# Optimization experiments

Measured on AMD Instinct MI355X. Metric: run time of the kernel, lower is better.

The kernel has to match this reference:

```python
import jax, jax.numpy as jnp
import numpy as np

B, CIN, COUT, H, W = 8, 64, 64, 128, 128
DG = 1          # deformable groups
K = 9           # 3x3 kernel taps


def conv2d(x, w, b, pad):
    out = jax.lax.conv_general_dilated(
        x, w, window_strides=(1, 1), padding=[(pad, pad), (pad, pad)],
        dimension_numbers=("NCHW", "OIHW", "NCHW"))
    return out + b[None, :, None, None]


def deform_conv2d(x, offset, w, b, dg):
    """torchvision-style DeformConv2d, 3x3, stride 1, pad 1, zeros outside."""
    Bn, Cin, Hn, Wn = x.shape
    Cout = w.shape[0]
    Cg = Cin // dg
    # offset: [B, 2*dg*K, H, W] -> [B, dg, K, 2, H, W] (dy, dx per tap)
    off = offset.reshape(Bn, dg, K, 2, Hn, Wn)
    ky = jnp.repeat(jnp.arange(3) - 1, 3).astype(x.dtype)   # [K]
    kx = jnp.tile(jnp.arange(3) - 1, 3).astype(x.dtype)     # [K]
    base_y = ky[:, None, None] + jnp.arange(Hn, dtype=x.dtype)[None, :, None]  # [K,H,1]
    base_x = kx[:, None, None] + jnp.arange(Wn, dtype=x.dtype)[None, None, :]  # [K,1,W]
    py = base_y[None, None] + off[:, :, :, 0]   # [B,dg,K,H,W]
    px = base_x[None, None] + off[:, :, :, 1]   # [B,dg,K,H,W]

    xg = x.reshape(Bn, dg, Cg, Hn * Wn)         # grouped, flat spatial
    y0 = jnp.floor(py)
    x0 = jnp.floor(px)
    acc = jnp.zeros((Bn, dg, Cg, K * Hn * Wn), dtype=x.dtype)
    for dy in (0, 1):
        for dx in (0, 1):
            yc = y0 + dy
            xc = x0 + dx
            # bilinear corner weight; |py-yc| <= 1 for the 4 corners
            wgt = (1.0 - jnp.abs(py - yc)) * (1.0 - jnp.abs(px - xc))
            valid = (yc >= 0) & (yc < Hn) & (xc >= 0) & (xc < Wn)
            yi = jnp.clip(yc, 0, Hn - 1).astype(jnp.int32)
            xi = jnp.clip(xc, 0, Wn - 1).astype(jnp.int32)
            idx = (yi * Wn + xi).reshape(Bn, dg, 1, -1)          # [B,dg,1,K*H*W]
            v = jnp.take_along_axis(xg, idx, axis=3)             # [B,dg,Cg,K*H*W]
            acc = acc + v * (wgt * valid.astype(x.dtype)).reshape(Bn, dg, 1, -1)
    sampled = acc.reshape(Bn, dg, Cg, K, Hn, Wn)
    wk = w.reshape(Cout, dg, Cg, K)              # [Cout,dg,Cg,K]
    out = jnp.einsum("bgckhw,ogck->bohw", sampled, wk)
    return out + b[None, :, None, None]


def setup_inputs() -> dict:
    key = jax.random.key(0)
    ks = jax.random.split(key, 12)
    s = 0.05  # weight scale to keep activations bounded through the relu stack
    inp = {
        "x": jax.random.normal(ks[0], (B, CIN, H, W), jnp.float32),
        "of": jax.random.normal(ks[1], (B, 2, H, W), jnp.float32),
        "w1": jax.random.normal(ks[2], (CIN, CIN, 3, 3), jnp.float32) * s,
        "b1": jnp.zeros((CIN,), jnp.float32),
        "w2": jax.random.normal(ks[3], (CIN, CIN, 3, 3), jnp.float32) * s,
        "b2": jnp.zeros((CIN,), jnp.float32),
        "w3": jax.random.normal(ks[4], (CIN, CIN, 3, 3), jnp.float32) * s,
        "b3": jnp.zeros((CIN,), jnp.float32),
        "w_off": jax.random.normal(ks[5], (K * DG * 2, 2, 1, 1), jnp.float32) * 0.1,
        "b_off": jnp.zeros((K * DG * 2,), jnp.float32),
        "w_d": jax.random.normal(ks[6], (COUT, CIN, 3, 3), jnp.float32) * s,
        "b_d": jnp.zeros((COUT,), jnp.float32),
    }
    return inp


def reference(x, of, w1, b1, w2, b2, w3, b3, w_off, b_off, w_d, b_d):
    h = jax.nn.relu(conv2d(x, w1, b1, 1))
    h = jax.nn.relu(conv2d(h, w2, b2, 1))
    h = jax.nn.relu(conv2d(h, w3, b3, 1))
    offset = conv2d(of, w_off, b_off, 0)          # 1x1 offset conv -> [B,18*dg,H,W]
    return deform_conv2d(h, offset, w_d, b_d, DG)
```

## Files before the change

### kernel.cpp

```cpp
#include <hip/hip_runtime.h>
#include <math.h>

#define H_ 128
#define W_ 128
#define B_ 8
#define C_ 64
#define HW_ (H_*W_)
#define PW 130

typedef _Float16 half8 __attribute__((ext_vector_type(8)));
typedef _Float16 half4t __attribute__((ext_vector_type(4)));
typedef float f32x4 __attribute__((ext_vector_type(4)));

__device__ __forceinline__ int clampi(int v, int lo, int hi) {
    return v < lo ? lo : (v > hi ? hi : v);
}

__device__ __forceinline__ void stage16(const _Float16* g, _Float16* l) {
    __builtin_amdgcn_global_load_lds(
        (const __attribute__((address_space(1))) unsigned int*)g,
        (__attribute__((address_space(3))) unsigned int*)l, 16, 0, 0);
}

__global__ __launch_bounds__(256, 4)
void prep_kernel(const float* __restrict__ w1, const float* __restrict__ w2,
                 const float* __restrict__ w3, const float* __restrict__ wd,
                 _Float16* __restrict__ wp,
                 _Float16* __restrict__ z0, _Float16* __restrict__ z1,
                 _Float16* __restrict__ z2,
                 const float* __restrict__ x,  _Float16* __restrict__ xp,
                 const float* __restrict__ of, const float* __restrict__ wof,
                 const float* __restrict__ bof, float* __restrict__ offb) {
    __shared__ float lds[64][129];
    const int blk = blockIdx.x;
    const int tid = threadIdx.x;

    if (blk < 72) {
        int t = blk * 256 + tid;
        if (t >= 4 * 4608) return;
        int set = t / 4608;
        int u   = t - set * 4608;
        const float* w = (set == 0) ? w1 : (set == 1) ? w2 : (set == 2) ? w3 : wd;
        int l  = u & 63;
        int mf = (u >> 6) & 3;
        int ch = (u >> 8) & 1;
        int kk = u >> 9;
        int co   = mf * 16 + (l & 15);
        int cin0 = ch * 32 + (l >> 4) * 8;
        half8 v;
#pragma unroll
        for (int j = 0; j < 8; ++j)
            v[j] = (_Float16)w[((co * C_) + cin0 + j) * 9 + kk];
        *(half8*)(wp + (size_t)set * 36864
                     + (size_t)(((ch * 9 + kk) * 4 + mf) * 64 + l) * 8) = v;
    } else if (blk < 121) {
        int t = (blk - 72) * 256 + tid;
        if (t >= 3 * B_ * 516) return;
        int which = t / (B_ * 516);
        int u = t - which * (B_ * 516);
        _Float16* o = (which == 0) ? z0 : (which == 1) ? z1 : z2;
        int b = u / 516, i = u % 516;
        int yp, xpx;
        if (i < 260) { yp = (i < 130) ? 0 : (PW - 1); xpx = i % 130; }
        else {
            int j = i - 260;
            if (j < 128) { xpx = 0; yp = j + 1; }
            else         { xpx = PW - 1; yp = j - 128 + 1; }
        }
        _Float16* dst = o + ((size_t)(b * PW + yp) * PW + xpx) * C_;
        half8 z = (half8)(_Float16)0.f;
#pragma unroll
        for (int c8 = 0; c8 < 8; ++c8) *(half8*)(dst + c8 * 8) = z;
    } else if (blk < 1145) {
        int bb = blk - 121;
        const int b = bb & 7, y = bb >> 3;
        const int xr = tid & 127, cr = tid >> 7;
        const float* src = x + (size_t)b * C_ * HW_ + y * W_;
#pragma unroll
        for (int i = 0; i < 32; ++i) {
            int c = i * 2 + cr;
            lds[c][xr] = src[(size_t)c * HW_ + xr];
        }
        __syncthreads();
        const int px = tid & 127, hf = tid >> 7;
        _Float16* dst = xp + ((size_t)((b * PW + y + 1) * PW) + px + 1) * C_ + hf * 32;
#pragma unroll
        for (int q = 0; q < 4; ++q) {
            half8 v;
#pragma unroll
            for (int j = 0; j < 8; ++j) v[j] = (_Float16)lds[hf * 32 + q * 8 + j][px];
            *(half8*)(dst + q * 8) = v;
        }
    } else {
        int bb = blk - 1145;
        int bi = bb & 7;
        int p  = (bb >> 3) * 256 + tid;
        float a0 = of[(bi * 2 + 0) * HW_ + p];
        float a1 = of[(bi * 2 + 1) * HW_ + p];
#pragma unroll
        for (int kk = 0; kk < 9; ++kk) {
            float dy = bof[2 * kk]     + wof[(2 * kk) * 2] * a0     + wof[(2 * kk) * 2 + 1] * a1;
            float dx = bof[2 * kk + 1] + wof[(2 * kk + 1) * 2] * a0 + wof[(2 * kk + 1) * 2 + 1] * a1;
            float2 v; v.x = dy; v.y = dx;
            *(float2*)(offb + ((size_t)(bi * 9 + kk) * HW_ + p) * 2) = v;
        }
    }
}

__global__ __launch_bounds__(256, 2)
void conv3x3_mfma(const _Float16* __restrict__ in, const _Float16* __restrict__ wpk,
                  const float* __restrict__ bias, _Float16* __restrict__ outp) {
    __shared__ _Float16 Ash[9 * 4 * 64 * 8];
    __shared__ _Float16 Tile[4 * 4 * 130 * 8];
    const int tid = threadIdx.x;
    const int wv = tid >> 6, l = tid & 63;
    const int l15 = l & 15, lg = l >> 4;
    const int b  = blockIdx.x & 7;
    const int R  = (blockIdx.x >> 3) * 2;
    const int rowi = wv >> 1;
    const int xcol = (wv & 1) * 64;

    f32x4 acc[4][4];
#pragma unroll
    for (int i = 0; i < 4; ++i)
#pragma unroll
        for (int j = 0; j < 4; ++j) acc[i][j] = (f32x4){0.f, 0.f, 0.f, 0.f};

    half8 bf0[4], bf1[4];

#define LOADB(BF, KK)                                                          \
    {                                                                          \
        _Pragma("unroll") for (int nf = 0; nf < 4; ++nf)                       \
            BF[nf] = *(const half8*)(Tile + (size_t)(((rowi + (KK) / 3) * 4 + lg) \
                          * 130 + xcol + (KK) % 3 + nf * 16 + l15) * 8);       \
    }
#define MM(BF, KK)                                                             \
    {                                                                          \
        half8 af_[4];                                                          \
        _Pragma("unroll") for (int mf = 0; mf < 4; ++mf)                       \
            af_[mf] = *(const half8*)(Ash + (size_t)(((KK) * 4 + mf) * 64 + l) * 8); \
        _Pragma("unroll") for (int mf = 0; mf < 4; ++mf)                       \
            _Pragma("unroll") for (int nf = 0; nf < 4; ++nf)                   \
                acc[mf][nf] = __builtin_amdgcn_mfma_f32_16x16x32_f16(          \
                    af_[mf], BF[nf], acc[mf][nf], 0, 0, 0);                    \
    }

#pragma unroll
    for (int ch = 0; ch < 2; ++ch) {
        __syncthreads();
#pragma unroll
        for (int i = 0; i < 18; ++i) {
            int idx = i * 256 + tid;
            if (idx < 2304) {
                stage16(wpk + (size_t)ch * 18432 + (size_t)idx * 8,
                        Ash + (size_t)idx * 8);
            } else if (idx < 4384) {
                int t   = idx - 2304;
                int dy  = t / 520;
                int rem = t - dy * 520;
                int pl  = rem / 130;
                int col = rem - pl * 130;
                stage16(in + ((size_t)((b * PW + R + dy) * PW) + col) * C_
                            + ch * 32 + pl * 8,
                        Tile + (size_t)t * 8);
            }
        }
        __syncthreads();

        LOADB(bf0, 0);
        LOADB(bf1, 1); MM(bf0, 0);
        LOADB(bf0, 2); MM(bf1, 1);
        LOADB(bf1, 3); MM(bf0, 2);
        LOADB(bf0, 4); MM(bf1, 3);
        LOADB(bf1, 5); MM(bf0, 4);
        LOADB(bf0, 6); MM(bf1, 5);
        LOADB(bf1, 7); MM(bf0, 6);
        LOADB(bf0, 8); MM(bf1, 7);
                       MM(bf0, 8);
    }
#undef LOADB
#undef MM

    _Float16* ob = outp + ((size_t)((b * PW + R + rowi + 1) * PW) + xcol + 1) * C_;
#pragma unroll
    for (int mf = 0; mf < 4; ++mf) {
        const int co = mf * 16 + lg * 4;
        const float b0 = bias[co], b1 = bias[co + 1], b2 = bias[co + 2], b3 = bias[co + 3];
#pragma unroll
        for (int nf = 0; nf < 4; ++nf) {
            f32x4 v = acc[mf][nf];
            half4t h;
            h[0] = (_Float16)fmaxf(v[0] + b0, 0.f);
            h[1] = (_Float16)fmaxf(v[1] + b1, 0.f);
            h[2] = (_Float16)fmaxf(v[2] + b2, 0.f);
            h[3] = (_Float16)fmaxf(v[3] + b3, 0.f);
            *(half4t*)(ob + (nf * 16 + l15) * C_ + co) = h;
        }
    }
}

__global__ __launch_bounds__(1024, 1)
void deform_mfma(const _Float16* __restrict__ hin, const float* __restrict__ off,
                 const _Float16* __restrict__ wpk, const float* __restrict__ bias,
                 float* __restrict__ out) {
    __shared__ _Float16 Ash[9 * 4 * 64 * 8];
    __shared__ _Float16 Win[8 * 130 * 40];
    __shared__ _Float16 OffS[9 * 4 * 128 * 4];
    const int tid = threadIdx.x;
    const int wv = tid >> 6, l = tid & 63;
    const int l15 = l & 15, lg = l >> 4;
    const int b  = blockIdx.x & 7;
    const int R  = (blockIdx.x >> 3) * 4;
    const int r  = R + (wv >> 2);
    const int xh = (wv & 3) * 32;

    const _Float16* hb = hin + (size_t)b * PW * PW * C_;
    const float* offp = off + (size_t)b * 9 * HW_ * 2;

#pragma unroll
    for (int i = 0; i < 3; ++i) {
        int idx = i * 1024 + tid;
        if (idx < 2304) {
            int kk = idx >> 8, rowi = (idx >> 6) & 3, c = idx & 63;
            const _Float16* g = (const _Float16*)(offp
                + ((size_t)kk * HW_ + (R + rowi) * W_) * 2) + c * 8;
            stage16(g, OffS + (size_t)idx * 8);
        }
    }

    f32x4 acc[4][2];
#pragma unroll
    for (int i = 0; i < 4; ++i)
#pragma unroll
        for (int j = 0; j < 2; ++j) acc[i][j] = (f32x4){0.f, 0.f, 0.f, 0.f};

    half8 bf[2];

#define GATHB(KK, CH) do {                                                     \
    _Pragma("unroll") for (int nf = 0; nf < 2; ++nf) {                         \
        const int pxl = xh + nf * 16 + l15;                                    \
        float2 o2 = *(const float2*)(OffS +                                    \
            (size_t)((((KK) * 4 + (r - R)) << 7) + pxl) * 4);                  \
        float py = (float)(r + (KK) / 3 - 1) + o2.x;                           \
        float px = (float)(pxl + (KK) % 3 - 1) + o2.y;                         \
        float fy0 = floorf(py), fx0 = floorf(px);                              \
        float fy = py - fy0, fx = px - fx0;                                    \
        int iy0 = (int)fy0, ix0 = (int)fx0;                                    \
        int cy0 = clampi(iy0, -1, 128), cy1 = clampi(iy0 + 1, -1, 128);        \
        int px0 = clampi(ix0, -1, 128) + 1, px1 = clampi(ix0 + 1, -1, 128) + 1;\
        _Float16 w00 = (_Float16)((1.f - fy) * (1.f - fx));                    \
        _Float16 w01 = (_Float16)((1.f - fy) * fx);                            \
        _Float16 w10 = (_Float16)(fy * (1.f - fx));                            \
        _Float16 w11 = (_Float16)(fy * fx);                                    \
        half8 c0, c1, c2, c3;                                                  \
        int s0 = cy0 + 2 - R, s1 = cy1 + 2 - R;                                \
        if (__all((s0 >= 0) & (s1 <= 7))) {                                    \
            const _Float16* w0 = Win + (size_t)(s0 * 130) * 40 + lg * 8;       \
            const _Float16* w1 = Win + (size_t)(s1 * 130) * 40 + lg * 8;       \
            c0 = *(const half8*)(w0 + px0 * 40);                               \
            c1 = *(const half8*)(w0 + px1 * 40);                               \
            c2 = *(const half8*)(w1 + px0 * 40);                               \
            c3 = *(const half8*)(w1 + px1 * 40);                               \
        } else {                                                               \
            const _Float16* g0 = hb + (size_t)((cy0 + 1) * PW) * C_ + (CH) * 32 + lg * 8; \
            const _Float16* g1 = hb + (size_t)((cy1 + 1) * PW) * C_ + (CH) * 32 + lg * 8; \
            c0 = *(const half8*)(g0 + px0 * C_);                               \
            c1 = *(const half8*)(g0 + px1 * C_);                               \
            c2 = *(const half8*)(g1 + px0 * C_);                               \
            c3 = *(const half8*)(g1 + px1 * C_);                               \
        }                                                                      \
        bf[nf] = (c0 * w00 + c1 * w01) + (c2 * w10 + c3 * w11);                \
    }                                                                          \
} while (0)
#define MMT(KK) do {                                                           \
    half8 af0 = *(const half8*)(Ash + (size_t)(((KK) * 4 + 0) * 64 + l) * 8);  \
    half8 af1 = *(const half8*)(Ash + (size_t)(((KK) * 4 + 1) * 64 + l) * 8);  \
    half8 af2 = *(const half8*)(Ash + (size_t)(((KK) * 4 + 2) * 64 + l) * 8);  \
    half8 af3 = *(const half8*)(Ash + (size_t)(((KK) * 4 + 3) * 64 + l) * 8);  \
    _Pragma("unroll") for (int nf = 0; nf < 2; ++nf) {                         \
        acc[0][nf] = __builtin_amdgcn_mfma_f32_16x16x32_f16(af0, bf[nf], acc[0][nf], 0, 0, 0); \
        acc[1][nf] = __builtin_amdgcn_mfma_f32_16x16x32_f16(af1, bf[nf], acc[1][nf], 0, 0, 0); \
        acc[2][nf] = __builtin_amdgcn_mfma_f32_16x16x32_f16(af2, bf[nf], acc[2][nf], 0, 0, 0); \
        acc[3][nf] = __builtin_amdgcn_mfma_f32_16x16x32_f16(af3, bf[nf], acc[3][nf], 0, 0, 0); \
    }                                                                          \
} while (0)

#pragma unroll
    for (int ch = 0; ch < 2; ++ch) {
        __syncthreads();
#pragma unroll
        for (int i = 0; i < 3; ++i) {
            int idx = i * 1024 + tid;
            if (idx < 2304)
                stage16(wpk + (size_t)ch * 18432 + (size_t)idx * 8,
                        Ash + (size_t)idx * 8);
        }
#pragma unroll
        for (int i = 0; i < 6; ++i) {
            int idx = i * 1024 + tid;
            if (idx < 5200) {
                int s   = idx / 650;
                int rem = idx - s * 650;
                int c   = rem / 5;
                int q   = rem - c * 5;
                int prow = clampi(R - 1 + s, 0, 129);
                stage16(hb + ((size_t)(prow * PW) + c) * C_ + ch * 32 + (q < 4 ? q : 3) * 8,
                        Win + (size_t)idx * 8);
            }
        }
        __syncthreads();

        GATHB(0, ch); MMT(0);
        GATHB(1, ch); MMT(1);
        GATHB(2, ch); MMT(2);
        GATHB(3, ch); MMT(3);
        GATHB(4, ch); MMT(4);
        GATHB(5, ch); MMT(5);
        GATHB(6, ch); MMT(6);
        GATHB(7, ch); MMT(7);
        GATHB(8, ch); MMT(8);
    }
#undef GATHB
#undef MMT

    float* WF = (float*)Win;
    float* obase = out + (size_t)b * C_ * HW_;
#pragma unroll
    for (int p = 0; p < 4; ++p) {
        __syncthreads();
#pragma unroll
        for (int nf = 0; nf < 2; ++nf) {
            f32x4 v = acc[p][nf];
#pragma unroll
            for (int rr = 0; rr < 4; ++rr) {
                int co16 = lg * 4 + rr;
                WF[co16 * 512 + (r - R) * 128 + xh + nf * 16 + l15]
                    = v[rr] + bias[p * 16 + co16];
            }
        }
        __syncthreads();
#pragma unroll
        for (int i = 0; i < 2; ++i) {
            int g4   = i * 1024 + tid;
            int co16 = g4 >> 7;
            int q    = g4 & 127;
            int rr2  = q >> 5;
            int px4  = q & 31;
            f32x4 v = *(const f32x4*)&WF[g4 * 4];
            *(f32x4*)(obase + (size_t)(p * 16 + co16) * HW_ + (R + rr2) * W_ + px4 * 4) = v;
        }
    }
}

extern "C" void kernel_launch(void* const* d_in, const int* in_sizes, int n_in,
                              void* d_out, int out_size, void* d_ws, size_t ws_size,
                              hipStream_t stream) {
    const float* x     = (const float*)d_in[0];
    const float* of    = (const float*)d_in[1];
    const float* w1    = (const float*)d_in[2];
    const float* b1    = (const float*)d_in[3];
    const float* w2    = (const float*)d_in[4];
    const float* b2    = (const float*)d_in[5];
    const float* w3    = (const float*)d_in[6];
    const float* b3    = (const float*)d_in[7];
    const float* w_off = (const float*)d_in[8];
    const float* b_off = (const float*)d_in[9];
    const float* w_d   = (const float*)d_in[10];
    const float* b_d   = (const float*)d_in[11];
    float* out = (float*)d_out;

    char* base = (char*)d_ws;
    float*     offb = (float*)base;
    char* p = base + (size_t)B_ * 18 * HW_ * 4;
    _Float16* wpA = (_Float16*)p;
    _Float16* wp1 = wpA;
    _Float16* wp2 = wp1 + 36864;
    _Float16* wp3 = wp2 + 36864;
    _Float16* wpd = wp3 + 36864;
    p += 4 * 36864 * 2;
    _Float16* xp = (_Float16*)p; p += (size_t)B_ * PW * PW * C_ * 2;
    _Float16* hA = (_Float16*)p; p += (size_t)B_ * PW * PW * C_ * 2;
    _Float16* hB = (_Float16*)p;

    prep_kernel<<<1657, 256, 0, stream>>>(w1, w2, w3, w_d, wpA,
                                          xp, hA, hB,
                                          x, xp, of, w_off, b_off, offb);

    conv3x3_mfma<<<512, 256, 0, stream>>>(xp, wp1, b1, hA);
    conv3x3_mfma<<<512, 256, 0, stream>>>(hA, wp2, b2, hB);
    conv3x3_mfma<<<512, 256, 0, stream>>>(hB, wp3, b3, hA);
    deform_mfma<<<256, 1024, 0, stream>>>(hA, offb, wpd, b_d, out);
}
```

Baseline: 103.6 us.

## Double-buffer LDS staging in conv3x3 to overlap second channel-half load with compute

The conv3x3 MFMA kernel now keeps two LDS buffers for weights and input tile. It issues the async global-to-LDS copy for the second channel half before computing the first half, which removes the barrier between the two halves. The goal is to hide the second stage's load latency inside one block. This doubles LDS use per block, so launch bounds drop to one block per CU, halving occupancy. With 512 blocks the grid may then need two waves instead of one.

```diff
diff --git a/kernel.cpp b/kernel.cpp
--- a/kernel.cpp
+++ b/kernel.cpp
@@ -107,11 +107,11 @@
     }
 }
 
-__global__ __launch_bounds__(256, 2)
+__global__ __launch_bounds__(256, 1)
 void conv3x3_mfma(const _Float16* __restrict__ in, const _Float16* __restrict__ wpk,
                   const float* __restrict__ bias, _Float16* __restrict__ outp) {
-    __shared__ _Float16 Ash[9 * 4 * 64 * 8];
-    __shared__ _Float16 Tile[4 * 4 * 130 * 8];
+    __shared__ _Float16 Ash[2][9 * 4 * 64 * 8];
+    __shared__ _Float16 Tile[2][4 * 4 * 130 * 8];
     const int tid = threadIdx.x;
     const int wv = tid >> 6, l = tid & 63;
     const int l15 = l & 15, lg = l >> 4;
@@ -128,58 +128,66 @@
 
     half8 bf0[4], bf1[4];
 
-#define LOADB(BF, KK)                                                          \
+#define STAGE(CH)                                                              \
+    {                                                                          \
+        _Pragma("unroll") for (int i = 0; i < 18; ++i) {                       \
+            int idx = i * 256 + tid;                                           \
+            if (idx < 2304) {                                                  \
+                stage16(wpk + (size_t)(CH) * 18432 + (size_t)idx * 8,          \
+                        Ash[CH] + (size_t)idx * 8);                            \
+            } else if (idx < 4384) {                                           \
+                int t   = idx - 2304;                                          \
+                int dy  = t / 520;                                             \
+                int rem = t - dy * 520;                                        \
+                int pl  = rem / 130;                                           \
+                int col = rem - pl * 130;                                      \
+                stage16(in + ((size_t)((b * PW + R + dy) * PW) + col) * C_     \
+                            + (CH) * 32 + pl * 8,                              \
+                        Tile[CH] + (size_t)t * 8);                             \
+            }                                                                  \
+        }                                                                      \
+    }
+#define LOADB(BF, KK, CH)                                                      \
     {                                                                          \
         _Pragma("unroll") for (int nf = 0; nf < 4; ++nf)                       \
-            BF[nf] = *(const half8*)(Tile + (size_t)(((rowi + (KK) / 3) * 4 + lg) \
+            BF[nf] = *(const half8*)(Tile[CH] + (size_t)(((rowi + (KK) / 3) * 4 + lg) \
                           * 130 + xcol + (KK) % 3 + nf * 16 + l15) * 8);       \
     }
-#define MM(BF, KK)                                                             \
+#define MM(BF, KK, CH)                                                         \
     {                                                                          \
         half8 af_[4];                                                          \
         _Pragma("unroll") for (int mf = 0; mf < 4; ++mf)                       \
-            af_[mf] = *(const half8*)(Ash + (size_t)(((KK) * 4 + mf) * 64 + l) * 8); \
+            af_[mf] = *(const half8*)(Ash[CH] + (size_t)(((KK) * 4 + mf) * 64 + l) * 8); \
         _Pragma("unroll") for (int mf = 0; mf < 4; ++mf)                       \
             _Pragma("unroll") for (int nf = 0; nf < 4; ++nf)                   \
                 acc[mf][nf] = __builtin_amdgcn_mfma_f32_16x16x32_f16(          \
                     af_[mf], BF[nf], acc[mf][nf], 0, 0, 0);                    \
     }
-
-#pragma unroll
-    for (int ch = 0; ch < 2; ++ch) {
-        __syncthreads();
-#pragma unroll
-        for (int i = 0; i < 18; ++i) {
-            int idx = i * 256 + tid;
-            if (idx < 2304) {
-                stage16(wpk + (size_t)ch * 18432 + (size_t)idx * 8,
-                        Ash + (size_t)idx * 8);
-            } else if (idx < 4384) {
-                int t   = idx - 2304;
-                int dy  = t / 520;
-                int rem = t - dy * 520;
-                int pl  = rem / 130;
-                int col = rem - pl * 130;
-                stage16(in + ((size_t)((b * PW + R + dy) * PW) + col) * C_
-                            + ch * 32 + pl * 8,
-                        Tile + (size_t)t * 8);
-            }
-        }
-        __syncthreads();
-
-        LOADB(bf0, 0);
-        LOADB(bf1, 1); MM(bf0, 0);
-        LOADB(bf0, 2); MM(bf1, 1);
-        LOADB(bf1, 3); MM(bf0, 2);
-        LOADB(bf0, 4); MM(bf1, 3);
-        LOADB(bf1, 5); MM(bf0, 4);
-        LOADB(bf0, 6); MM(bf1, 5);
-        LOADB(bf1, 7); MM(bf0, 6);
-        LOADB(bf0, 8); MM(bf1, 7);
-                       MM(bf0, 8);
-    }
+#define COMPUTE(CH)                                                            \
+    {                                                                          \
+        LOADB(bf0, 0, CH);                                                     \
+        LOADB(bf1, 1, CH); MM(bf0, 0, CH);                                     \
+        LOADB(bf0, 2, CH); MM(bf1, 1, CH);                                     \
+        LOADB(bf1, 3, CH); MM(bf0, 2, CH);                                     \
+        LOADB(bf0, 4, CH); MM(bf1, 3, CH);                                     \
+        LOADB(bf1, 5, CH); MM(bf0, 4, CH);                                     \
+        LOADB(bf0, 6, CH); MM(bf1, 5, CH);                                     \
+        LOADB(bf1, 7, CH); MM(bf0, 6, CH);                                     \
+        LOADB(bf0, 8, CH); MM(bf1, 7, CH);                                     \
+                           MM(bf0, 8, CH);                                     \
+    }
+
+    STAGE(0);
+    __syncthreads();
+    STAGE(1);
+    COMPUTE(0);
+    __syncthreads();
+    COMPUTE(1);
+
+#undef STAGE
 #undef LOADB
 #undef MM
+#undef COMPUTE
 
     _Float16* ob = outp + ((size_t)((b * PW + R + rowi + 1) * PW) + xcol + 1) * C_;
 #pragma unroll
```

New measurement: 107.4 us. 3.6% more time.
